# Kernel tuning notes

Measured on AMD Instinct MI355X. Metric: run time of the kernel, lower is better.

Reference implementation:

```python
import jax, jax.numpy as jnp
import numpy as np

T, D = 4096, 1536          # tokens, hidden
H, KV, HD = 24, 8, 64      # heads, kv heads, head dim
E, TOPK, F = 32, 8, 512    # experts, top-k, expert intermediate
FS = 1024                  # shared-MLP intermediate
THETA = 10000.0
AMULT = 0.015625           # attention_multiplier (replaces 1/sqrt(hd))
RMULT = 0.22               # residual_multiplier
EPS = 1e-6


def setup_inputs() -> dict:
    key = jax.random.key(0)
    ks = jax.random.split(key, 12)
    s = 0.02
    return {
        'positions': jnp.arange(T, dtype=jnp.int32),
        'hidden_states': jax.random.normal(ks[0], (T, D), jnp.float32),
        'ln1_w': jnp.ones((D,), jnp.float32),
        'wq': jax.random.normal(ks[1], (D, H * HD), jnp.float32) * s,
        'wk': jax.random.normal(ks[2], (D, KV * HD), jnp.float32) * s,
        'wv': jax.random.normal(ks[3], (D, KV * HD), jnp.float32) * s,
        'wo': jax.random.normal(ks[4], (H * HD, D), jnp.float32) * s,
        'ln2_w': jnp.ones((D,), jnp.float32),
        'router_w': jax.random.normal(ks[5], (D, E), jnp.float32) * s,
        'w_gate_up': jax.random.normal(ks[6], (E, D, 2 * F), jnp.float32) * s,
        'w_down': jax.random.normal(ks[7], (E, F, D), jnp.float32) * s,
        'shared_gate_up': jax.random.normal(ks[8], (D, 2 * FS), jnp.float32) * s,
        'shared_down': jax.random.normal(ks[9], (FS, D), jnp.float32) * s,
    }


def _rmsnorm(x, w):
    var = jnp.mean(x * x, axis=-1, keepdims=True)
    return x * jax.lax.rsqrt(var + EPS) * w


def _rope(x, positions):
    # x: [T, nH, HD], neox-style half rotation
    half = HD // 2
    inv_freq = 1.0 / (THETA ** (jnp.arange(half, dtype=jnp.float32) / half))
    ang = positions.astype(jnp.float32)[:, None] * inv_freq[None, :]  # [T, half]
    cos, sin = jnp.cos(ang)[:, None, :], jnp.sin(ang)[:, None, :]
    x1, x2 = x[..., :half], x[..., half:]
    return jnp.concatenate([x1 * cos - x2 * sin, x2 * cos + x1 * sin], axis=-1)


def _silu_and_mul(gu):
    g, u = jnp.split(gu, 2, axis=-1)
    return jax.nn.silu(g) * u


def reference(positions, hidden_states, ln1_w, wq, wk, wv, wo, ln2_w,
              router_w, w_gate_up, w_down, shared_gate_up, shared_down):
    # ---- attention block ----
    residual = hidden_states
    h = _rmsnorm(hidden_states, ln1_w)
    q = _rope((h @ wq).reshape(T, H, HD), positions)
    k = _rope((h @ wk).reshape(T, KV, HD), positions)
    v = (h @ wv).reshape(T, KV, HD)
    k = jnp.repeat(k, H // KV, axis=1)  # GQA expand -> [T, H, HD]
    v = jnp.repeat(v, H // KV, axis=1)
    scores = jnp.einsum('thd,shd->hts', q, k) * AMULT
    mask = jnp.tril(jnp.ones((T, T), dtype=bool))
    scores = jnp.where(mask[None], scores, jnp.finfo(scores.dtype).min)
    probs = jax.nn.softmax(scores, axis=-1)
    attn = jnp.einsum('hts,shd->thd', probs, v).reshape(T, H * HD) @ wo
    hidden = residual + attn * RMULT

    # ---- MoE + shared MLP block ----
    residual = hidden
    h = _rmsnorm(hidden, ln2_w)
    # router: top-k logits, softmax over selected (renormalized gates)
    logits = h @ router_w                          # [T, E]
    topv, topi = jax.lax.top_k(logits, TOPK)       # [T, TOPK]
    gates = jax.nn.softmax(topv, axis=-1)
    # per-token dense expert weight map [T, E] (zero for unselected experts)
    wmap = jnp.sum(jax.nn.one_hot(topi, E, dtype=h.dtype) * gates[..., None], axis=1)
    gu = jnp.einsum('td,edf->tef', h, w_gate_up)   # [T, E, 2F]
    act = _silu_and_mul(gu)                        # [T, E, F]
    moe_out = jnp.einsum('tef,efd,te->td', act, w_down, wmap)
    # shared SiLU MLP
    shared = _silu_and_mul(h @ shared_gate_up) @ shared_down
    hidden = residual + (moe_out + shared) * RMULT
    return hidden
```

## Files before the change

### kernel.cpp

```cpp
#include <hip/hip_runtime.h>
#include <stdint.h>

using u16 = unsigned short;
using u32 = unsigned int;

typedef __attribute__((ext_vector_type(8))) short short8;
typedef __attribute__((ext_vector_type(4))) short short4v;
typedef __attribute__((ext_vector_type(4))) float f32x4;

#define MFMA16(a,b,c) __builtin_amdgcn_mfma_f32_16x16x32_bf16(a,b,c,0,0,0)

__device__ __forceinline__ u16 f2bf(float f){
  u32 u = __float_as_uint(f);
  u += 0x7fffu + ((u>>16)&1u);
  return (u16)(u>>16);
}
__device__ __forceinline__ float bf2f(u16 b){ return __uint_as_float(((u32)b)<<16); }

__device__ __forceinline__ void gload16(const void* g, void* l){
  __builtin_amdgcn_global_load_lds(
      (const __attribute__((address_space(1))) u32*)g,
      (__attribute__((address_space(3))) u32*)l, 16, 0, 0);
}

__device__ __forceinline__ float red16_max(float x){
  float r;
  asm("v_max_f32 %0, %1, %1 row_ror:8 row_mask:0xf bank_mask:0xf" : "=v"(r) : "v"(x));
  asm("v_max_f32 %0, %1, %1 row_ror:4 row_mask:0xf bank_mask:0xf" : "=v"(r) : "v"(r));
  asm("v_max_f32 %0, %1, %1 row_ror:2 row_mask:0xf bank_mask:0xf" : "=v"(r) : "v"(r));
  asm("v_max_f32 %0, %1, %1 row_ror:1 row_mask:0xf bank_mask:0xf" : "=v"(r) : "v"(r));
  return r;
}
__device__ __forceinline__ float red16_sum(float x){
  float r;
  asm("v_add_f32 %0, %1, %1 row_ror:8 row_mask:0xf bank_mask:0xf" : "=v"(r) : "v"(x));
  asm("v_add_f32 %0, %1, %1 row_ror:4 row_mask:0xf bank_mask:0xf" : "=v"(r) : "v"(r));
  asm("v_add_f32 %0, %1, %1 row_ror:2 row_mask:0xf bank_mask:0xf" : "=v"(r) : "v"(r));
  asm("v_add_f32 %0, %1, %1 row_ror:1 row_mask:0xf bank_mask:0xf" : "=v"(r) : "v"(r));
  return r;
}

__global__ __launch_bounds__(256) void k_wt(const float* __restrict__ src,
    u16* __restrict__ dst, int K, int N, long sstride, long dstride)
{
  __shared__ float tile[32][33];
  int nb = blockIdx.x*32, kb = blockIdx.y*32;
  const float* S = src + (long)blockIdx.z*sstride;
  u16* D = dst + (long)blockIdx.z*dstride;
  int tid = threadIdx.x;
  int r = tid>>3, c4 = (tid&7)*4;
  f32x4 v = *(const f32x4*)&S[(long)(kb+r)*N + nb + c4];
  tile[r][c4+0]=v[0]; tile[r][c4+1]=v[1]; tile[r][c4+2]=v[2]; tile[r][c4+3]=v[3];
  __syncthreads();
  short4v o;
  o[0]=(short)f2bf(tile[c4+0][r]);
  o[1]=(short)f2bf(tile[c4+1][r]);
  o[2]=(short)f2bf(tile[c4+2][r]);
  o[3]=(short)f2bf(tile[c4+3][r]);
  *(short4v*)&D[(long)(nb+r)*K + kb + c4] = o;
}

__global__ __launch_bounds__(256) void k_wti(const float* __restrict__ src,
    u16* __restrict__ dst, int K, int N, int halfN, long sstride, long dstride)
{
  __shared__ float tile[32][33];
  int nb = blockIdx.x*32, kb = blockIdx.y*32;
  const float* S = src + (long)blockIdx.z*sstride;
  u16* D = dst + (long)blockIdx.z*dstride;
  int tid = threadIdx.x;
  int r = tid>>3, c4 = (tid&7)*4;
  int scol = (nb>>1) + (c4&15) + ((c4&16)? halfN : 0);
  f32x4 v = *(const f32x4*)&S[(long)(kb+r)*N + scol];
  tile[r][c4+0]=v[0]; tile[r][c4+1]=v[1]; tile[r][c4+2]=v[2]; tile[r][c4+3]=v[3];
  __syncthreads();
  short4v o;
  o[0]=(short)f2bf(tile[c4+0][r]);
  o[1]=(short)f2bf(tile[c4+1][r]);
  o[2]=(short)f2bf(tile[c4+2][r]);
  o[3]=(short)f2bf(tile[c4+3][r]);
  *(short4v*)&D[(long)(nb+r)*K + kb + c4] = o;
}

__global__ __launch_bounds__(256) void k_vt(const u16* __restrict__ v,
                                            u16* __restrict__ vT)
{
  __shared__ u16 t_[64*72];
  int t0 = blockIdx.x*64, kvh = blockIdx.y;
  int tid = threadIdx.x;
  #pragma unroll
  for (int i=0;i<2;++i){
    int c = tid + i*256;
    int row = c>>3, dc = (c&7)*8;
    *(short8*)&t_[row*72 + dc] = *(const short8*)&v[(long)(t0+row)*2560 + kvh*64 + dc];
  }
  __syncthreads();
  #pragma unroll
  for (int i=0;i<2;++i){
    int c = tid + i*256;
    int d = c>>3, tc = (c&7)*8;
    short8 o;
    #pragma unroll
    for (int j=0;j<8;++j) o[j] = (short)t_[(tc+j)*72 + d];
    *(short8*)&vT[(long)(kvh*64 + d)*4096 + t0 + tc] = o;
  }
}

__global__ __launch_bounds__(192) void k_rmsnorm(const float* __restrict__ x,
                                                 const float* __restrict__ w,
                                                 u16* __restrict__ o)
{
  int t = blockIdx.x, tid = threadIdx.x;
  const float* xr = x + (size_t)t*1536 + tid*8;
  f32x4 a = *(const f32x4*)xr;
  f32x4 b = *(const f32x4*)(xr+4);
  float ss = a[0]*a[0]+a[1]*a[1]+a[2]*a[2]+a[3]*a[3]
           + b[0]*b[0]+b[1]*b[1]+b[2]*b[2]+b[3]*b[3];
  #pragma unroll
  for (int m=1;m<64;m<<=1) ss += __shfl_xor(ss,m);
  __shared__ float red[3];
  if ((tid&63)==0) red[tid>>6]=ss;
  __syncthreads();
  float inv = rsqrtf((red[0]+red[1]+red[2])*(1.0f/1536.0f)+1e-6f);
  const float* wp = w + tid*8;
  f32x4 wa = *(const f32x4*)wp;
  f32x4 wb = *(const f32x4*)(wp+4);
  u16* op = o + (size_t)t*1536 + tid*8;
  #pragma unroll
  for (int j=0;j<4;++j) op[j]   = f2bf(a[j]*inv*wa[j]);
  #pragma unroll
  for (int j=0;j<4;++j) op[j+4] = f2bf(b[j]*inv*wb[j]);
}

template<int MODE, int GATHER>
__global__ __launch_bounds__(256,3) void k_gemm(
    const u16* __restrict__ A, int lda,
    const u16* __restrict__ Bt, long strideB, int K,
    int Mfix, const int* __restrict__ cnts, const int* __restrict__ offs,
    const int* __restrict__ toks, const float* __restrict__ gates,
    u16* __restrict__ Cb, int ldcb,
    float* __restrict__ Cf, int ldcf,
    const float* __restrict__ resid)
{
  int e = blockIdx.z;
  int M = cnts ? cnts[e] : Mfix;
  int m0 = blockIdx.y*128;
  if (m0 >= M) return;
  int roff = offs ? offs[e] : 0;
  const u16* Bp = Bt + (long)e*strideB;
  int col0 = blockIdx.x*128;

  __shared__ u16 Ash[4096];
  __shared__ u16 Bsh[4096];

  int tid = threadIdx.x, wv = tid>>6, lane = tid&63;
  int lr = lane&15, lg = lane>>4;
  int wr = (wv>>1)*64, wc = (wv&1)*64;

  int row0 = tid>>2, kc = (tid&3)*8;
  int gr0 = min(m0 + row0,      M-1);
  int gr1 = min(m0 + row0 + 64, M-1);
  int ar0, ar1;
  if (GATHER){ ar0 = toks[roff + gr0]; ar1 = toks[roff + gr1]; }
  else       { ar0 = roff + gr0;       ar1 = roff + gr1; }
  const u16* ap0 = A + (long)ar0*lda + kc;
  const u16* ap1 = A + (long)ar1*lda + kc;
  const u16* bp0 = Bp + (long)(col0 + row0)*K + kc;
  const u16* bp1 = bp0 + (long)64*K;

  u16* As0 = &Ash[wv*512];  u16* As1 = &Ash[2048 + wv*512];
  u16* Bs0 = &Bsh[wv*512];  u16* Bs1 = &Bsh[2048 + wv*512];

  f32x4 acc[4][4];
  #pragma unroll
  for (int m=0;m<4;++m)
    #pragma unroll
    for (int n=0;n<4;++n)
      acc[m][n] = (f32x4){0.f,0.f,0.f,0.f};

  int nk = K>>5;
  for (int kt=0; kt<nk; ++kt){
    __syncthreads();
    gload16(ap0, As0); gload16(ap1, As1);
    gload16(bp0, Bs0); gload16(bp1, Bs1);
    ap0 += 32; ap1 += 32; bp0 += 32; bp1 += 32;
    __syncthreads();

    short8 af[4], b1[4];
    #pragma unroll
    for (int m=0;m<4;++m) af[m] = *(const short8*)&Ash[(wr+m*16+lr)*32 + lg*8];
    #pragma unroll
    for (int n=0;n<4;++n) b1[n] = *(const short8*)&Bsh[(wc+n*16+lr)*32 + lg*8];
    #pragma unroll
    for (int m=0;m<4;++m)
      #pragma unroll
      for (int n=0;n<4;++n)
        acc[m][n] = MFMA16(af[m], b1[n], acc[m][n]);
  }

  if constexpr(MODE==6){
    #pragma unroll
    for (int m=0;m<4;++m)
      #pragma unroll
      for (int np=0;np<2;++np)
        #pragma unroll
        for (int rr=0;rr<4;++rr){
          int row = wr + m*16 + lg*4 + rr;
          int gr = m0 + row;
          if (gr >= M) continue;
          float g = acc[m][2*np][rr];
          float u = acc[m][2*np+1][rr];
          float s = g/(1.f+__expf(-g))*u;
          int j = (wc>>1) + np*16 + lr;
          Cb[(long)(roff+gr)*ldcb + (col0>>1) + j] = f2bf(s);
        }
  } else {
    #pragma unroll
    for (int m=0;m<4;++m)
      #pragma unroll
      for (int n=0;n<4;++n)
        #pragma unroll
        for (int rr=0;rr<4;++rr){
          int row = wr + m*16 + lg*4 + rr;
          int gr = m0 + row;
          if (gr >= M) continue;
          int col = wc + n*16 + lr;
          float va = acc[m][n][rr];
          if constexpr(MODE==0){
            Cb[(long)(roff+gr)*ldcb + col0 + col] = f2bf(va);
          } else if constexpr(MODE==1){
            long idx = (long)gr*ldcf + col0 + col;
            Cf[idx] = resid[idx] + va*0.22f;
          } else if constexpr(MODE==5){
            float gt = gates[roff+gr];
            Cb[(long)(roff+gr)*ldcb + col0 + col] = f2bf(va*gt);
          }
        }
  }
}

__global__ __launch_bounds__(192) void k_moesum(const u16* __restrict__ part,
    const int* __restrict__ inv, float* __restrict__ out)
{
  int t = blockIdx.x, tid = threadIdx.x;
  int c = tid*8;
  float s[8] = {0.f,0.f,0.f,0.f,0.f,0.f,0.f,0.f};
  #pragma unroll
  for (int kk=0;kk<8;++kk){
    int slot = inv[t*8+kk];
    short8 v = *(const short8*)&part[(long)slot*1536 + c];
    #pragma unroll
    for (int j=0;j<8;++j) s[j] += bf2f((u16)v[j]);
  }
  float* op = out + (long)t*1536 + c;
  f32x4 o0 = *(const f32x4*)op;
  f32x4 o1 = *(const f32x4*)(op+4);
  #pragma unroll
  for (int j=0;j<4;++j){ o0[j] += s[j]; o1[j] += s[j+4]; }
  *(f32x4*)op = o0;
  *(f32x4*)(op+4) = o1;
}

__global__ __launch_bounds__(256) void k_rope(const int* __restrict__ pos,
    u16* __restrict__ qkvb)
{
  int gid = blockIdx.x*256 + threadIdx.x;
  int t = gid >> 10, p = gid & 1023;
  int j = p & 31;
  float invf = __expf(-(float)j * 0.28782313662425574f);
  float ang = (float)pos[t] * invf;
  float sn, cs; __sincosf(ang, &sn, &cs);
  u16* base;
  if (p < 768) base = qkvb + (long)t*2560 + (p>>5)*64;
  else         base = qkvb + (long)t*2560 + 1536 + ((p-768)>>5)*64;
  float x1 = bf2f(base[j]), x2 = bf2f(base[j+32]);
  base[j]    = f2bf(x1*cs - x2*sn);
  base[j+32] = f2bf(x2*cs + x1*sn);
}

__global__ __launch_bounds__(256,3) void k_attn(const u16* __restrict__ qg,
    const u16* __restrict__ kg, const u16* __restrict__ vT,
    u16* __restrict__ og, u16* __restrict__ Opart, float* __restrict__ mlb)
{
  int bid = blockIdx.x;
  int kvh = bid & 7;
  int ii = bid >> 3;
  int qt, kt0, kt1, chunk; bool single;
  if (ii < 32)      { qt = 32+ii;        chunk = 0; kt0 = 0;  kt1 = 32;   single = false; }
  else if (ii < 64) { qt = 63-(ii-32);   chunk = 1; kt0 = 32; kt1 = qt+1; single = false; }
  else              { qt = 31-(ii-64);   chunk = 0; kt0 = 0;  kt1 = qt+1; single = true;  }

  int tid = threadIdx.x, wv = tid>>6, lane = tid&63;
  int lr = lane&15, lg = lane>>4;
  __shared__ u16 Ksh[64*72];
  __shared__ u16 Vsh[64*72];
  __shared__ u16 Psh[4][16*72];
  int q0 = qt*64;
  int qrow = q0 + wv*16 + lr;
  short8 qf[3][2];
  #pragma unroll
  for (int hh=0;hh<3;++hh)
    #pragma unroll
    for (int c=0;c<2;++c)
      qf[hh][c] = *(const short8*)&qg[(long)qrow*2560 + (kvh*3+hh)*64 + c*32 + lg*8];

  float m_[3][4], l_[3][4];
  f32x4 Ot[3][4];
  #pragma unroll
  for (int hh=0;hh<3;++hh)
    #pragma unroll
    for (int r=0;r<4;++r){ m_[hh][r]=-1e30f; l_[hh][r]=0.f; }
  #pragma unroll
  for (int hh=0;hh<3;++hh)
    #pragma unroll
    for (int d=0;d<4;++d) Ot[hh][d]=(f32x4){0.f,0.f,0.f,0.f};

  int srow = tid>>3, sdc = (tid&7)*8;
  short8 kreg[2], vreg[2];
  auto loadKV = [&](int kt){
    #pragma unroll
    for (int i=0;i<2;++i){
      int row = srow + i*32;
      kreg[i] = *(const short8*)&kg[(long)(kt*64+row)*2560 + kvh*64 + sdc];
      vreg[i] = *(const short8*)&vT[(long)(kvh*64 + row)*4096 + kt*64 + sdc];
    }
  };
  loadKV(kt0);

  for (int kt=kt0; kt<kt1; ++kt){
    __syncthreads();
    #pragma unroll
    for (int i=0;i<2;++i){
      int row = srow + i*32;
      *(short8*)&Ksh[row*72 + sdc] = kreg[i];
      *(short8*)&Vsh[row*72 + sdc] = vreg[i];
    }
    __syncthreads();
    if (kt < kt1-1) loadKV(kt+1);
    bool diag = (kt==qt);

    #pragma unroll
    for (int hh=0;hh<3;++hh){
      f32x4 S[4];
      #pragma unroll
      for (int n=0;n<4;++n) S[n]=(f32x4){0.f,0.f,0.f,0.f};
      #pragma unroll
      for (int n=0;n<4;++n)
        #pragma unroll
        for (int c=0;c<2;++c){
          short8 kf = *(const short8*)&Ksh[(n*16+lr)*72 + c*32 + lg*8];
          S[n] = MFMA16(qf[hh][c], kf, S[n]);
        }

      float rmax[4] = {-1e30f,-1e30f,-1e30f,-1e30f};
      #pragma unroll
      for (int n=0;n<4;++n)
        #pragma unroll
        for (int r=0;r<4;++r){
          float sv = S[n][r]*0.015625f;
          if (diag){
            int colg = n*16 + lr;
            int rowg = wv*16 + lg*4 + r;
            if (colg > rowg) sv = -1e30f;
          }
          S[n][r] = sv;
          rmax[r] = fmaxf(rmax[r], sv);
        }
      #pragma unroll
      for (int r=0;r<4;++r) rmax[r] = red16_max(rmax[r]);

      float alpha[4], rsum[4];
      #pragma unroll
      for (int r=0;r<4;++r){
        float mn = fmaxf(m_[hh][r], rmax[r]);
        alpha[r] = __expf(m_[hh][r]-mn);
        m_[hh][r] = mn;
        rsum[r] = 0.f;
      }
      #pragma unroll
      for (int n=0;n<4;++n)
        #pragma unroll
        for (int r=0;r<4;++r){
          float pv = __expf(S[n][r]-m_[hh][r]);
          S[n][r]=pv; rsum[r]+=pv;
        }
      #pragma unroll
      for (int r=0;r<4;++r) rsum[r] = red16_sum(rsum[r]);
      #pragma unroll
      for (int r=0;r<4;++r) l_[hh][r] = l_[hh][r]*alpha[r] + rsum[r];
      #pragma unroll
      for (int d=0;d<4;++d)
        #pragma unroll
        for (int r=0;r<4;++r) Ot[hh][d][r] *= alpha[r];

      #pragma unroll
      for (int n=0;n<4;++n)
        #pragma unroll
        for (int r=0;r<4;++r)
          Psh[wv][(lg*4+r)*72 + n*16 + lr] = f2bf(S[n][r]);
      #pragma unroll
      for (int c=0;c<2;++c){
        short8 pf = *(const short8*)&Psh[wv][lr*72 + c*32 + lg*8];
        #pragma unroll
        for (int d=0;d<4;++d){
          short8 vf = *(const short8*)&Vsh[(d*16+lr)*72 + c*32 + lg*8];
          Ot[hh][d] = MFMA16(pf, vf, Ot[hh][d]);
        }
      }
    }
  }

  if (single){
    #pragma unroll
    for (int hh=0;hh<3;++hh)
      #pragma unroll
      for (int d=0;d<4;++d)
        #pragma unroll
        for (int r=0;r<4;++r){
          int t = q0 + wv*16 + lg*4 + r;
          og[(long)t*1536 + (kvh*3+hh)*64 + d*16 + lr] = f2bf(Ot[hh][d][r]/l_[hh][r]);
        }
  } else {
    #pragma unroll
    for (int hh=0;hh<3;++hh){
      int h = kvh*3+hh;
      #pragma unroll
      for (int r=0;r<4;++r){
        int t = q0 + wv*16 + lg*4 + r;
        long slot = ((long)(t-2048)*24 + h)*2 + chunk;
        #pragma unroll
        for (int d=0;d<4;++d)
          Opart[slot*64 + d*16 + lr] = f2bf(Ot[hh][d][r]);
        if (lr==0){ mlb[slot*2] = m_[hh][r]; mlb[slot*2+1] = l_[hh][r]; }
      }
    }
  }
}

__global__ __launch_bounds__(256) void k_comb(const u16* __restrict__ Opart,
    const float* __restrict__ mlb, u16* __restrict__ og)
{
  int gid = blockIdx.x*256 + threadIdx.x;
  int d = gid & 63;
  long rowi = gid >> 6;
  long s0 = rowi*2, s1 = s0+1;
  float m0 = mlb[s0*2], l0 = mlb[s0*2+1];
  float m1 = mlb[s1*2], l1 = mlb[s1*2+1];
  float M = fmaxf(m0,m1);
  float w0 = __expf(m0-M), w1 = __expf(m1-M);
  float o = (bf2f(Opart[s0*64+d])*w0 + bf2f(Opart[s1*64+d])*w1) / (l0*w0 + l1*w1);
  int t = 2048 + (int)(rowi/24), h = (int)(rowi - (rowi/24)*24);
  og[(long)t*1536 + h*64 + d] = f2bf(o);
}

__global__ __launch_bounds__(64) void k_router(const u16* __restrict__ h2,
    const float* __restrict__ rw, int* __restrict__ topi, float* __restrict__ gatev)
{
  int t = blockIdx.x, lane = threadIdx.x;
  int e = lane & 31, hf = lane >> 5;
  const u16* hr = h2 + (size_t)t*1536 + hf*768;
  const float* wp = rw + (long)hf*768*32 + e;
  float s = 0.f;
  for (int d=0; d<768; ++d)
    s += bf2f(hr[d]) * wp[(long)d*32];
  s += __shfl_xor(s, 32);
  __shared__ float lgt[32];
  if (lane < 32) lgt[e] = s;
  __syncthreads();
  if (lane==0){
    u32 msk=0; float tv[8]; int ti[8];
    for (int kk=0;kk<8;++kk){
      float best=-1e30f; int bi=0;
      for (int j2=0;j2<32;++j2)
        if (!((msk>>j2)&1u) && lgt[j2] > best){ best=lgt[j2]; bi=j2; }
      msk |= 1u<<bi; tv[kk]=best; ti[kk]=bi;
    }
    float mx = tv[0], ssum = 0.f, ge[8];
    for (int kk=0;kk<8;++kk){ ge[kk]=__expf(tv[kk]-mx); ssum+=ge[kk]; }
    float isum = 1.f/ssum;
    for (int kk=0;kk<8;++kk){ topi[t*8+kk]=ti[kk]; gatev[t*8+kk]=ge[kk]*isum; }
  }
}

__global__ void k_hist(const int* __restrict__ topi, int* __restrict__ cnt){
  int i = blockIdx.x*256 + threadIdx.x;
  if (i < 4096*8) atomicAdd(&cnt[topi[i]], 1);
}
__global__ void k_scan(const int* __restrict__ cnt, int* __restrict__ offs, int* __restrict__ cur){
  if (threadIdx.x==0 && blockIdx.x==0){
    int a=0;
    for (int e2=0;e2<32;++e2){ offs[e2]=a; cur[e2]=a; a+=cnt[e2]; }
  }
}
__global__ void k_scatter(const int* __restrict__ topi, const float* __restrict__ gatev,
    int* __restrict__ cur, int* __restrict__ toks, float* __restrict__ gts,
    int* __restrict__ inv){
  int i = blockIdx.x*256 + threadIdx.x;
  if (i < 4096*8){
    int e2 = topi[i];
    int p = atomicAdd(&cur[e2], 1);
    toks[p] = i>>3;
    gts[p] = gatev[i]*0.22f;
    inv[i] = p;
  }
}

extern "C" void kernel_launch(void* const* d_in, const int* in_sizes, int n_in,
                              void* d_out, int out_size, void* d_ws, size_t ws_size,
                              hipStream_t stream)
{
  const int*   positions = (const int*)  d_in[0];
  const float* hs   = (const float*)d_in[1];
  const float* ln1w = (const float*)d_in[2];
  const float* wq   = (const float*)d_in[3];
  const float* wk   = (const float*)d_in[4];
  const float* wv   = (const float*)d_in[5];
  const float* wo   = (const float*)d_in[6];
  const float* ln2w = (const float*)d_in[7];
  const float* rww  = (const float*)d_in[8];
  const float* wgu  = (const float*)d_in[9];
  const float* wdn  = (const float*)d_in[10];
  const float* sgu  = (const float*)d_in[11];
  const float* sdn  = (const float*)d_in[12];
  float* out = (float*)d_out;

  char* ws = (char*)d_ws;
  size_t off = 0;
  auto alloc = [&](size_t b)->void*{ void* p = ws + off; off += (b + 255) & ~(size_t)255; return p; };

  u16* hbf     = (u16*)alloc((size_t)4096*1536*2);
  u16* qkv     = (u16*)alloc((size_t)33554432);
  u16* qkvb = qkv;
  u16* aout = qkv + (size_t)4096*2560;
  u16* act_moe = qkv;
  u16* act_sh  = (u16*)alloc((size_t)4096*1024*2);
  u16* vT      = (u16*)alloc((size_t)8*64*4096*2);
  int*   topi  = (int*)  alloc(4096*8*4);
  float* gatev = (float*)alloc(4096*8*4);
  int*   toks  = (int*)  alloc(4096*8*4);
  float* gts   = (float*)alloc(4096*8*4);
  int*   inv   = (int*)  alloc(4096*8*4);
  int*   cnt   = (int*)  alloc(512);
  int*   offs  = (int*)  alloc(512);
  int*   cur   = (int*)  alloc(512);
  u16* wqkvT = (u16*)alloc((size_t)2560*1536*2);
  u16* woT  = (u16*)alloc((size_t)1536*1536*2);
  u16* sguT = (u16*)alloc((size_t)2048*1536*2);
  u16* sdnT = (u16*)alloc((size_t)1536*1024*2);
  u16* wguT = (u16*)alloc((size_t)32*1024*1536*2);
  u16* wdnT = (u16*)alloc((size_t)32*1536*512*2);
  float* hidden2 = out;
  u16*   h2bf = hbf;
  u16*   Opart = hbf;
  float* mlb   = (float*)act_sh;
  u16*   part  = wguT;

  k_wt <<<dim3(48,48,1), 256,0,stream>>>(wq,  wqkvT,               1536,1536, 0,0);
  k_wt <<<dim3(16,48,1), 256,0,stream>>>(wk,  wqkvT+(size_t)1536*1536, 1536,512, 0,0);
  k_wt <<<dim3(16,48,1), 256,0,stream>>>(wv,  wqkvT+(size_t)2048*1536, 1536,512, 0,0);
  k_wt <<<dim3(48,48,1), 256,0,stream>>>(wo,  woT,  1536,1536, 0,0);
  k_wti<<<dim3(64,48,1), 256,0,stream>>>(sgu, sguT, 1536,2048,1024, 0,0);
  k_wt <<<dim3(48,32,1), 256,0,stream>>>(sdn, sdnT, 1024,1536, 0,0);
  k_wti<<<dim3(32,48,32),256,0,stream>>>(wgu, wguT, 1536,1024,512, (long)1536*1024, (long)1536*1024);
  k_wt <<<dim3(48,16,32),256,0,stream>>>(wdn, wdnT, 512,1536,  (long)512*1536,  (long)512*1536);

  k_rmsnorm<<<4096,192,0,stream>>>(hs, ln1w, hbf);
  k_gemm<0,0><<<dim3(20,32,1),256,0,stream>>>(hbf,1536, wqkvT,0,1536, 4096,nullptr,nullptr,nullptr,nullptr, qkvb,2560, nullptr,0, nullptr);
  k_rope<<<16384,256,0,stream>>>(positions, qkvb);
  k_vt<<<dim3(64,8,1),256,0,stream>>>(qkvb + 2048, vT);
  k_attn<<<dim3(768,1,1),256,0,stream>>>(qkvb, qkvb + 1536, vT, aout, Opart, mlb);
  k_comb<<<12288,256,0,stream>>>(Opart, mlb, aout);
  k_gemm<1,0><<<dim3(12,32,1),256,0,stream>>>(aout,1536, woT,0,1536, 4096,nullptr,nullptr,nullptr,nullptr, nullptr,0, hidden2,1536, hs);
  k_rmsnorm<<<4096,192,0,stream>>>(hidden2, ln2w, h2bf);
  k_router<<<4096,64,0,stream>>>(h2bf, rww, topi, gatev);
  hipMemsetAsync(cnt, 0, 32*4, stream);
  k_hist<<<128,256,0,stream>>>(topi, cnt);
  k_scan<<<1,64,0,stream>>>(cnt, offs, cur);
  k_scatter<<<128,256,0,stream>>>(topi, gatev, cur, toks, gts, inv);
  k_gemm<6,1><<<dim3(8,32,32),256,0,stream>>>(h2bf,1536, wguT,(long)1024*1536,1536, 0,cnt,offs,toks,nullptr, act_moe,512, nullptr,0, nullptr);
  k_gemm<6,0><<<dim3(16,32,1),256,0,stream>>>(h2bf,1536, sguT,0,1536, 4096,nullptr,nullptr,nullptr,nullptr, act_sh,1024, nullptr,0, nullptr);
  k_gemm<1,0><<<dim3(12,32,1),256,0,stream>>>(act_sh,1024, sdnT,0,1024, 4096,nullptr,nullptr,nullptr,nullptr, nullptr,0, out,1536, out);
  k_gemm<5,0><<<dim3(12,32,32),256,0,stream>>>(act_moe,512, wdnT,(long)1536*512,512, 0,cnt,offs,nullptr,gts, part,1536, nullptr,0, nullptr);
  k_moesum<<<4096,192,0,stream>>>(part, inv, out);

  (void)in_sizes; (void)n_in; (void)out_size; (void)ws_size;
}
```

Measured before the change: 1.025 ms.

## Fuse RoPE into QKV GEMM epilogue, fold histogram into router, enlarge transpose tiles

RoPE moves into a new QKV GEMM epilogue (MODE 7) that rotates the Q/K columns in registers before writing bf16, so the separate k_rope pass that reread and rewrote qkvb is gone. The expert histogram is now counted with atomics inside the router, removing the k_hist launch. The weight transpose/convert kernels use 64x64 tiles with four loads per thread instead of 32x32, cutting block count. The risks are more atomic contention in the router and a sincos per element in the GEMM epilogue.

```diff
diff --git a/kernel.cpp b/kernel.cpp
--- a/kernel.cpp
+++ b/kernel.cpp
@@ -9,6 +9,7 @@
 typedef __attribute__((ext_vector_type(4))) float f32x4;
 
 #define MFMA16(a,b,c) __builtin_amdgcn_mfma_f32_16x16x32_bf16(a,b,c,0,0,0)
+
 
 __device__ __forceinline__ u16 f2bf(float f){
   u32 u = __float_as_uint(f);
@@ -43,42 +44,54 @@
 __global__ __launch_bounds__(256) void k_wt(const float* __restrict__ src,
     u16* __restrict__ dst, int K, int N, long sstride, long dstride)
 {
-  __shared__ float tile[32][33];
-  int nb = blockIdx.x*32, kb = blockIdx.y*32;
+  __shared__ float tile[64][65];
+  int nb = blockIdx.x*64, kb = blockIdx.y*64;
   const float* S = src + (long)blockIdx.z*sstride;
   u16* D = dst + (long)blockIdx.z*dstride;
   int tid = threadIdx.x;
-  int r = tid>>3, c4 = (tid&7)*4;
-  f32x4 v = *(const f32x4*)&S[(long)(kb+r)*N + nb + c4];
-  tile[r][c4+0]=v[0]; tile[r][c4+1]=v[1]; tile[r][c4+2]=v[2]; tile[r][c4+3]=v[3];
+  int rr = tid>>4, c4 = (tid&15)*4;
+  #pragma unroll
+  for (int p=0;p<4;++p){
+    int r = p*16 + rr;
+    f32x4 v = *(const f32x4*)&S[(long)(kb+r)*N + nb + c4];
+    tile[r][c4+0]=v[0]; tile[r][c4+1]=v[1]; tile[r][c4+2]=v[2]; tile[r][c4+3]=v[3];
+  }
   __syncthreads();
-  short4v o;
-  o[0]=(short)f2bf(tile[c4+0][r]);
-  o[1]=(short)f2bf(tile[c4+1][r]);
-  o[2]=(short)f2bf(tile[c4+2][r]);
-  o[3]=(short)f2bf(tile[c4+3][r]);
-  *(short4v*)&D[(long)(nb+r)*K + kb + c4] = o;
+  #pragma unroll
+  for (int p=0;p<4;++p){
+    int nn = p*16 + rr;
+    short4v o;
+    #pragma unroll
+    for (int i=0;i<4;++i) o[i] = (short)f2bf(tile[c4+i][nn]);
+    *(short4v*)&D[(long)(nb+nn)*K + kb + c4] = o;
+  }
 }
 
 __global__ __launch_bounds__(256) void k_wti(const float* __restrict__ src,
     u16* __restrict__ dst, int K, int N, int halfN, long sstride, long dstride)
 {
-  __shared__ float tile[32][33];
-  int nb = blockIdx.x*32, kb = blockIdx.y*32;
+  __shared__ float tile[64][65];
+  int nb = blockIdx.x*64, kb = blockIdx.y*64;
   const float* S = src + (long)blockIdx.z*sstride;
   u16* D = dst + (long)blockIdx.z*dstride;
   int tid = threadIdx.x;
-  int r = tid>>3, c4 = (tid&7)*4;
-  int scol = (nb>>1) + (c4&15) + ((c4&16)? halfN : 0);
-  f32x4 v = *(const f32x4*)&S[(long)(kb+r)*N + scol];
-  tile[r][c4+0]=v[0]; tile[r][c4+1]=v[1]; tile[r][c4+2]=v[2]; tile[r][c4+3]=v[3];
+  int rr = tid>>4, c4 = (tid&15)*4;
+  int scol = (nb>>1) + ((c4>>5)<<4) + (c4&15) + (((c4>>4)&1)? halfN : 0);
+  #pragma unroll
+  for (int p=0;p<4;++p){
+    int r = p*16 + rr;
+    f32x4 v = *(const f32x4*)&S[(long)(kb+r)*N + scol];
+    tile[r][c4+0]=v[0]; tile[r][c4+1]=v[1]; tile[r][c4+2]=v[2]; tile[r][c4+3]=v[3];
+  }
   __syncthreads();
-  short4v o;
-  o[0]=(short)f2bf(tile[c4+0][r]);
-  o[1]=(short)f2bf(tile[c4+1][r]);
-  o[2]=(short)f2bf(tile[c4+2][r]);
-  o[3]=(short)f2bf(tile[c4+3][r]);
-  *(short4v*)&D[(long)(nb+r)*K + kb + c4] = o;
+  #pragma unroll
+  for (int p=0;p<4;++p){
+    int nn = p*16 + rr;
+    short4v o;
+    #pragma unroll
+    for (int i=0;i<4;++i) o[i] = (short)f2bf(tile[c4+i][nn]);
+    *(short4v*)&D[(long)(nb+nn)*K + kb + c4] = o;
+  }
 }
 
 __global__ __launch_bounds__(256) void k_vt(const u16* __restrict__ v,
@@ -139,7 +152,7 @@
     const int* __restrict__ toks, const float* __restrict__ gates,
     u16* __restrict__ Cb, int ldcb,
     float* __restrict__ Cf, int ldcf,
-    const float* __restrict__ resid)
+    const float* __restrict__ resid, const int* __restrict__ pos)
 {
   int e = blockIdx.z;
   int M = cnts ? cnts[e] : Mfix;
@@ -213,6 +226,38 @@
           int j = (wc>>1) + np*16 + lr;
           Cb[(long)(roff+gr)*ldcb + (col0>>1) + j] = f2bf(s);
         }
+  } else if constexpr(MODE==7){
+    if (col0 < 2048){
+      float invf0 = __expf(-(float)lr      * 0.28782313662425574f);
+      float invf1 = __expf(-(float)(lr+16) * 0.28782313662425574f);
+      #pragma unroll
+      for (int m=0;m<4;++m)
+        #pragma unroll
+        for (int rr=0;rr<4;++rr){
+          int gr = m0 + wr + m*16 + lg*4 + rr;
+          float pv = (float)pos[gr];
+          #pragma unroll
+          for (int n=0;n<2;++n){
+            float sn, cs;
+            __sincosf(pv * (n ? invf1 : invf0), &sn, &cs);
+            float x1 = acc[m][n][rr], x2 = acc[m][n+2][rr];
+            long base = (long)gr*ldcb + col0 + wc + n*16 + lr;
+            Cb[base]      = f2bf(x1*cs - x2*sn);
+            Cb[base + 32] = f2bf(x2*cs + x1*sn);
+          }
+        }
+    } else {
+      #pragma unroll
+      for (int m=0;m<4;++m)
+        #pragma unroll
+        for (int n=0;n<4;++n)
+          #pragma unroll
+          for (int rr=0;rr<4;++rr){
+            int gr = m0 + wr + m*16 + lg*4 + rr;
+            int col = wc + n*16 + lr;
+            Cb[(long)gr*ldcb + col0 + col] = f2bf(acc[m][n][rr]);
+          }
+    }
   } else {
     #pragma unroll
     for (int m=0;m<4;++m)
@@ -260,23 +305,6 @@
   *(f32x4*)(op+4) = o1;
 }
 
-__global__ __launch_bounds__(256) void k_rope(const int* __restrict__ pos,
-    u16* __restrict__ qkvb)
-{
-  int gid = blockIdx.x*256 + threadIdx.x;
-  int t = gid >> 10, p = gid & 1023;
-  int j = p & 31;
-  float invf = __expf(-(float)j * 0.28782313662425574f);
-  float ang = (float)pos[t] * invf;
-  float sn, cs; __sincosf(ang, &sn, &cs);
-  u16* base;
-  if (p < 768) base = qkvb + (long)t*2560 + (p>>5)*64;
-  else         base = qkvb + (long)t*2560 + 1536 + ((p-768)>>5)*64;
-  float x1 = bf2f(base[j]), x2 = bf2f(base[j+32]);
-  base[j]    = f2bf(x1*cs - x2*sn);
-  base[j+32] = f2bf(x2*cs + x1*sn);
-}
-
 __global__ __launch_bounds__(256,3) void k_attn(const u16* __restrict__ qg,
     const u16* __restrict__ kg, const u16* __restrict__ vT,
     u16* __restrict__ og, u16* __restrict__ Opart, float* __restrict__ mlb)
@@ -453,7 +481,8 @@
 }
 
 __global__ __launch_bounds__(64) void k_router(const u16* __restrict__ h2,
-    const float* __restrict__ rw, int* __restrict__ topi, float* __restrict__ gatev)
+    const float* __restrict__ rw, int* __restrict__ topi, float* __restrict__ gatev,
+    int* __restrict__ cnt)
 {
   int t = blockIdx.x, lane = threadIdx.x;
   int e = lane & 31, hf = lane >> 5;
@@ -477,14 +506,13 @@
     float mx = tv[0], ssum = 0.f, ge[8];
     for (int kk=0;kk<8;++kk){ ge[kk]=__expf(tv[kk]-mx); ssum+=ge[kk]; }
     float isum = 1.f/ssum;
-    for (int kk=0;kk<8;++kk){ topi[t*8+kk]=ti[kk]; gatev[t*8+kk]=ge[kk]*isum; }
-  }
-}
-
-__global__ void k_hist(const int* __restrict__ topi, int* __restrict__ cnt){
-  int i = blockIdx.x*256 + threadIdx.x;
-  if (i < 4096*8) atomicAdd(&cnt[topi[i]], 1);
-}
+    for (int kk=0;kk<8;++kk){
+      topi[t*8+kk]=ti[kk]; gatev[t*8+kk]=ge[kk]*isum;
+      atomicAdd(&cnt[ti[kk]], 1);
+    }
+  }
+}
+
 __global__ void k_scan(const int* __restrict__ cnt, int* __restrict__ offs, int* __restrict__ cur){
   if (threadIdx.x==0 && blockIdx.x==0){
     int a=0;
@@ -554,32 +582,30 @@
   float* mlb   = (float*)act_sh;
   u16*   part  = wguT;
 
-  k_wt <<<dim3(48,48,1), 256,0,stream>>>(wq,  wqkvT,               1536,1536, 0,0);
-  k_wt <<<dim3(16,48,1), 256,0,stream>>>(wk,  wqkvT+(size_t)1536*1536, 1536,512, 0,0);
-  k_wt <<<dim3(16,48,1), 256,0,stream>>>(wv,  wqkvT+(size_t)2048*1536, 1536,512, 0,0);
-  k_wt <<<dim3(48,48,1), 256,0,stream>>>(wo,  woT,  1536,1536, 0,0);
-  k_wti<<<dim3(64,48,1), 256,0,stream>>>(sgu, sguT, 1536,2048,1024, 0,0);
-  k_wt <<<dim3(48,32,1), 256,0,stream>>>(sdn, sdnT, 1024,1536, 0,0);
-  k_wti<<<dim3(32,48,32),256,0,stream>>>(wgu, wguT, 1536,1024,512, (long)1536*1024, (long)1536*1024);
-  k_wt <<<dim3(48,16,32),256,0,stream>>>(wdn, wdnT, 512,1536,  (long)512*1536,  (long)512*1536);
+  k_wt <<<dim3(24,24,1), 256,0,stream>>>(wq,  wqkvT,                   1536,1536, 0,0);
+  k_wt <<<dim3(8,24,1),  256,0,stream>>>(wk,  wqkvT+(size_t)1536*1536, 1536,512,  0,0);
+  k_wt <<<dim3(8,24,1),  256,0,stream>>>(wv,  wqkvT+(size_t)2048*1536, 1536,512,  0,0);
+  k_wt <<<dim3(24,24,1), 256,0,stream>>>(wo,  woT,  1536,1536, 0,0);
+  k_wti<<<dim3(32,24,1), 256,0,stream>>>(sgu, sguT, 1536,2048,1024, 0,0);
+  k_wt <<<dim3(24,16,1), 256,0,stream>>>(sdn, sdnT, 1024,1536, 0,0);
+  k_wti<<<dim3(16,24,32),256,0,stream>>>(wgu, wguT, 1536,1024,512, (long)1536*1024, (long)1536*1024);
+  k_wt <<<dim3(24,8,32), 256,0,stream>>>(wdn, wdnT, 512,1536,  (long)512*1536,  (long)512*1536);
 
   k_rmsnorm<<<4096,192,0,stream>>>(hs, ln1w, hbf);
-  k_gemm<0,0><<<dim3(20,32,1),256,0,stream>>>(hbf,1536, wqkvT,0,1536, 4096,nullptr,nullptr,nullptr,nullptr, qkvb,2560, nullptr,0, nullptr);
-  k_rope<<<16384,256,0,stream>>>(positions, qkvb);
+  k_gemm<7,0><<<dim3(20,32,1),256,0,stream>>>(hbf,1536, wqkvT,0,1536, 4096,nullptr,nullptr,nullptr,nullptr, qkvb,2560, nullptr,0, nullptr, positions);
   k_vt<<<dim3(64,8,1),256,0,stream>>>(qkvb + 2048, vT);
   k_attn<<<dim3(768,1,1),256,0,stream>>>(qkvb, qkvb + 1536, vT, aout, Opart, mlb);
   k_comb<<<12288,256,0,stream>>>(Opart, mlb, aout);
-  k_gemm<1,0><<<dim3(12,32,1),256,0,stream>>>(aout,1536, woT,0,1536, 4096,nullptr,nullptr,nullptr,nullptr, nullptr,0, hidden2,1536, hs);
+  k_gemm<1,0><<<dim3(12,32,1),256,0,stream>>>(aout,1536, woT,0,1536, 4096,nullptr,nullptr,nullptr,nullptr, nullptr,0, hidden2,1536, hs, nullptr);
   k_rmsnorm<<<4096,192,0,stream>>>(hidden2, ln2w, h2bf);
-  k_router<<<4096,64,0,stream>>>(h2bf, rww, topi, gatev);
   hipMemsetAsync(cnt, 0, 32*4, stream);
-  k_hist<<<128,256,0,stream>>>(topi, cnt);
+  k_router<<<4096,64,0,stream>>>(h2bf, rww, topi, gatev, cnt);
   k_scan<<<1,64,0,stream>>>(cnt, offs, cur);
   k_scatter<<<128,256,0,stream>>>(topi, gatev, cur, toks, gts, inv);
-  k_gemm<6,1><<<dim3(8,32,32),256,0,stream>>>(h2bf,1536, wguT,(long)1024*1536,1536, 0,cnt,offs,toks,nullptr, act_moe,512, nullptr,0, nullptr);
-  k_gemm<6,0><<<dim3(16,32,1),256,0,stream>>>(h2bf,1536, sguT,0,1536, 4096,nullptr,nullptr,nullptr,nullptr, act_sh,1024, nullptr,0, nullptr);
-  k_gemm<1,0><<<dim3(12,32,1),256,0,stream>>>(act_sh,1024, sdnT,0,1024, 4096,nullptr,nullptr,nullptr,nullptr, nullptr,0, out,1536, out);
-  k_gemm<5,0><<<dim3(12,32,32),256,0,stream>>>(act_moe,512, wdnT,(long)1536*512,512, 0,cnt,offs,nullptr,gts, part,1536, nullptr,0, nullptr);
+  k_gemm<6,1><<<dim3(8,32,32),256,0,stream>>>(h2bf,1536, wguT,(long)1024*1536,1536, 0,cnt,offs,toks,nullptr, act_moe,512, nullptr,0, nullptr, nullptr);
+  k_gemm<6,0><<<dim3(16,32,1),256,0,stream>>>(h2bf,1536, sguT,0,1536, 4096,nullptr,nullptr,nullptr,nullptr, act_sh,1024, nullptr,0, nullptr, nullptr);
+  k_gemm<1,0><<<dim3(12,32,1),256,0,stream>>>(act_sh,1024, sdnT,0,1024, 4096,nullptr,nullptr,nullptr,nullptr, nullptr,0, out,1536, out, nullptr);
+  k_gemm<5,0><<<dim3(12,32,32),256,0,stream>>>(act_moe,512, wdnT,(long)1536*512,512, 0,cnt,offs,nullptr,gts, part,1536, nullptr,0, nullptr, nullptr);
   k_moesum<<<4096,192,0,stream>>>(part, inv, out);
 
   (void)in_sizes; (void)n_in; (void)out_size; (void)ws_size;
```

After: 1.113 ms. 1.09x slower.
